# Optimization experiments

Hardware: AMD Instinct MI355X
Metric: run time of the kernel (lower is better)

Reference implementation:

```python
import jax, jax.numpy as jnp
import numpy as np

DIM = 1280
N_HEADS = 10
HEAD_DIM = 128
BASE = 10000.0
BATCH = 2
SEQ = 2048


def _rope(x):
    # x: [b, h, s, d]; matches source: split even/odd channels, rotate, concat halves
    b, h, s, d = x.shape
    theta = 1.0 / (BASE ** (jnp.arange(0, d, 2, dtype=jnp.float32) / d))  # [d/2]
    ang = jnp.arange(s, dtype=jnp.float32)[:, None] * theta               # [s, d/2]
    cos = jnp.cos(ang)
    sin = jnp.sin(ang)
    x1 = x[..., 0::2]
    x2 = x[..., 1::2]
    return jnp.concatenate([x1 * cos - x2 * sin, x1 * sin + x2 * cos], axis=-1)


def setup_inputs() -> dict:
    key = jax.random.key(0)
    ks = jax.random.split(key, 6)
    w_std = 0.02
    x = jax.random.normal(ks[0], (BATCH, SEQ, DIM), dtype=jnp.float32)
    positions = jnp.arange(SEQ, dtype=jnp.int64 if jax.config.jax_enable_x64 else jnp.int32)
    Wq = jax.random.normal(ks[1], (DIM, DIM), dtype=jnp.float32) * w_std
    Wk = jax.random.normal(ks[2], (DIM, DIM), dtype=jnp.float32) * w_std
    Wv = jax.random.normal(ks[3], (DIM, DIM), dtype=jnp.float32) * w_std
    Wo = jax.random.normal(ks[4], (DIM, DIM), dtype=jnp.float32) * w_std
    bq = jnp.zeros((DIM,), jnp.float32)
    bk = jnp.zeros((DIM,), jnp.float32)
    bv = jnp.zeros((DIM,), jnp.float32)
    bo = jnp.zeros((DIM,), jnp.float32)
    return {"x": x, "positions": positions, "Wq": Wq, "bq": bq, "Wk": Wk,
            "bk": bk, "Wv": Wv, "bv": bv, "Wo": Wo, "bo": bo}


def reference(x, positions, Wq, bq, Wk, bk, Wv, bv, Wo, bo):
    b, s, _ = x.shape
    scale = 1.0 / np.sqrt(HEAD_DIM)

    def proj(W, bias):
        y = jnp.einsum('bsd,ed->bse', x, W) + bias  # Linear: x @ W^T + b
        return y.reshape(b, s, N_HEADS, HEAD_DIM).transpose(0, 2, 1, 3)

    q = _rope(proj(Wq, bq))  # [b, h, s, hd]
    k = _rope(proj(Wk, bk))
    v = proj(Wv, bv)

    scores = jnp.einsum('bhqd,bhkd->bhqk', q, k) * scale
    causal = jnp.tril(jnp.ones((s, s), dtype=bool))
    scores = jnp.where(causal, scores, jnp.float32(-jnp.inf))
    attn = jax.nn.softmax(scores, axis=-1)
    out = jnp.einsum('bhqk,bhkd->bhqd', attn, v)
    out = out.transpose(0, 2, 1, 3).reshape(b, s, N_HEADS * HEAD_DIM)
    return jnp.einsum('bse,de->bsd', out, Wo) + bo
```

## Files before the change

kernel.cpp:

```cpp
#include <hip/hip_runtime.h>
#include <cmath>

typedef unsigned short u16;
typedef __attribute__((ext_vector_type(8))) short bf16x8;
typedef __attribute__((ext_vector_type(4))) float f32x4;

#define B_    2
#define SEQ_  2048
#define NH_   10
#define HD_   128
#define DIM_  1280

__device__ __forceinline__ u16 f2bf(float f) {
    union { float f; unsigned u; } v; v.f = f;
    unsigned r = (v.u + 0x7fffu + ((v.u >> 16) & 1u)) >> 16;
    return (u16)r;
}
__device__ __forceinline__ float bf2f(u16 h) {
    union { unsigned u; float f; } v; v.u = ((unsigned)h) << 16;
    return v.f;
}
__device__ __forceinline__ f32x4 mfma16(bf16x8 a, bf16x8 b, f32x4 c) {
    return __builtin_amdgcn_mfma_f32_16x16x32_bf16(a, b, c, 0, 0, 0);
}
__device__ __forceinline__ void g2l16(const void* g, void* l) {
    __builtin_amdgcn_global_load_lds(
        (const __attribute__((address_space(1))) unsigned*)g,
        (__attribute__((address_space(3))) unsigned*)l, 16, 0, 0);
}
__device__ __forceinline__ ushort4 pack4(float a, float b, float c, float d) {
    ushort4 w; w.x = f2bf(a); w.y = f2bf(b); w.z = f2bf(c); w.w = f2bf(d);
    return w;
}
__device__ __forceinline__ bf16x8 ldsr128(unsigned byte_off) {
    bf16x8 r;
    asm volatile("ds_read_b128 %0, %1" : "=v"(r) : "v"(byte_off));
    return r;
}
__device__ __forceinline__ unsigned lds_off(const void* p) {
    return (unsigned)(unsigned long long)
        (__attribute__((address_space(3))) const void*)p;
}

#define LGKM0() do { asm volatile("s_waitcnt lgkmcnt(0)" ::: "memory"); \
                     __builtin_amdgcn_sched_barrier(0); } while (0)
#define VMC(n)  asm volatile("s_waitcnt vmcnt(" #n ")" ::: "memory")

__global__ __launch_bounds__(256) void cvt_k(const float* __restrict__ x,
                                             const float* __restrict__ w0,
                                             const float* __restrict__ w1,
                                             const float* __restrict__ w2,
                                             const float* __restrict__ w3,
                                             u16* __restrict__ xb,
                                             u16* __restrict__ d0,
                                             u16* __restrict__ d1,
                                             u16* __restrict__ d2,
                                             u16* __restrict__ d3,
                                             float* __restrict__ ct,
                                             float* __restrict__ st) {
    const int NX = B_ * SEQ_ * DIM_;
    const int WN = DIM_ * DIM_;
    const int NCV = (NX + 4 * WN) / 8 / 256;
    int bid = blockIdx.x;
    if (bid >= NCV) {
        int idx = (bid - NCV) * 256 + threadIdx.x;
        int s = idx >> 6, j = idx & 63;
        float e = (float)j * (1.0f / 64.0f);
        float theta = 1.0f / powf(10000.0f, e);
        float ang = (float)s * theta;
        ct[idx] = cosf(ang);
        st[idx] = sinf(ang);
        return;
    }
    int i = (bid * 256 + threadIdx.x) * 8;
    const float* src; u16* dst; int off;
    if (i < NX) { src = x; dst = xb; off = i; }
    else {
        int j = i - NX; int w = j / WN; off = j - w * WN;
        src = (w == 0) ? w0 : (w == 1) ? w1 : (w == 2) ? w2 : w3;
        dst = (w == 0) ? d0 : (w == 1) ? d1 : (w == 2) ? d2 : d3;
    }
    float4 a0 = *(const float4*)(src + off);
    float4 a1 = *(const float4*)(src + off + 4);
    union { uint4 q; u16 u[8]; } t;
    t.u[0] = f2bf(a0.x); t.u[1] = f2bf(a0.y);
    t.u[2] = f2bf(a0.z); t.u[3] = f2bf(a0.w);
    t.u[4] = f2bf(a1.x); t.u[5] = f2bf(a1.y);
    t.u[6] = f2bf(a1.z); t.u[7] = f2bf(a1.w);
    *(uint4*)(dst + off) = t.q;
}

template <typename OT>
__device__ __forceinline__ void gemm_core(const u16* __restrict__ A,
                                          const u16* __restrict__ W,
                                          const float* __restrict__ bias,
                                          OT* __restrict__ C,
                                          int m_blk, int n_blk,
                                          u16* As, u16* Bs) {
    const int tid = threadIdx.x;
    const int wave = tid >> 6, lane = tid & 63;
    const int quad = lane >> 4, l16 = lane & 15;
    const int w_m = (wave >> 1) * 64, w_n = (wave & 1) * 64;
    const int srow = wave * 32;
    const int lrow = lane >> 3;
    const int csw = ((lane & 7) ^ lrow) * 8;
    const int rsw = l16 & 7;
    f32x4 acc[4][4] = {};

    const u16* pa = A + (size_t)(m_blk + srow + lrow) * DIM_ + csw;
    const u16* pb = W + (size_t)(n_blk + srow + lrow) * DIM_ + csw;

    for (int k0 = 0; k0 < DIM_; k0 += 64) {
        #pragma unroll
        for (int i = 0; i < 4; ++i) {
            g2l16(pa + k0 + i * 8 * DIM_, As + (srow + i * 8) * 64);
            g2l16(pb + k0 + i * 8 * DIM_, Bs + (srow + i * 8) * 64);
        }
        __syncthreads();
        #pragma unroll
        for (int kk = 0; kk < 2; ++kk) {
            bf16x8 af[4], bf[4];
            #pragma unroll
            for (int mt = 0; mt < 4; ++mt)
                af[mt] = *(const bf16x8*)&As[(w_m + mt * 16 + l16) * 64
                                             + ((kk * 4 + quad) ^ rsw) * 8];
            #pragma unroll
            for (int nt = 0; nt < 4; ++nt)
                bf[nt] = *(const bf16x8*)&Bs[(w_n + nt * 16 + l16) * 64
                                             + ((kk * 4 + quad) ^ rsw) * 8];
            #pragma unroll
            for (int mt = 0; mt < 4; ++mt)
                #pragma unroll
                for (int nt = 0; nt < 4; ++nt)
                    acc[mt][nt] = mfma16(af[mt], bf[nt], acc[mt][nt]);
        }
        __syncthreads();
    }
    #pragma unroll
    for (int nt = 0; nt < 4; ++nt) {
        int col = n_blk + w_n + nt * 16 + l16;
        float bv = bias[col];
        #pragma unroll
        for (int mt = 0; mt < 4; ++mt) {
            #pragma unroll
            for (int r = 0; r < 4; ++r) {
                int row = m_blk + w_m + mt * 16 + quad * 4 + r;
                float v = acc[mt][nt][r] + bv;
                if constexpr (sizeof(OT) == 4) C[(size_t)row * DIM_ + col] = v;
                else C[(size_t)row * DIM_ + col] = (OT)f2bf(v);
            }
        }
    }
}

__device__ __forceinline__ void gemm256_core(const u16* __restrict__ A,
                                             const u16* __restrict__ W,
                                             const float* __restrict__ bias,
                                             u16* __restrict__ C,
                                             int m_blk, int n_blk,
                                             u16* sm) {
    const int tid = threadIdx.x;
    const int wave = tid >> 6, lane = tid & 63;
    const int quad = lane >> 4, l16 = lane & 15;
    const int wr = wave >> 2, wc = wave & 3;
    const int rsw = (l16 >> 1) & 3;
    const unsigned smb = lds_off(sm);
    const unsigned aB = smb + ((wr * 128 + l16) * 32 + (quad ^ rsw) * 8) * 2;
    const unsigned bB = smb + (16384 + (wc * 64 + l16) * 32 + (quad ^ rsw) * 8) * 2;
    const int csw = ((lane & 3) ^ ((lane >> 3) & 3)) * 8;
    const int jA = wave * 2, jB = wave * 2 + 1;
    const int kkA = jA >> 3, gA0 = jA & 7;
    const int kkB = jB >> 3, gB0 = jB & 7;
    const u16* pa = A + (size_t)(m_blk + (lane >> 2)) * DIM_ + csw;
    const u16* pb = W + (size_t)(n_blk + (lane >> 2)) * DIM_ + csw;

    #define STG(p, mat, d, h, tk) do {                                        \
        int g0_ = gA0 + (h) * 8, g1_ = gB0 + (h) * 8;                         \
        g2l16((p) + (size_t)(g0_ * 16) * DIM_ + (tk) * 64 + kkA * 32,         \
              sm + (d) * 32768 + (mat) * 16384 + kkA * 8192 + g0_ * 512);     \
        g2l16((p) + (size_t)(g1_ * 16) * DIM_ + (tk) * 64 + kkB * 32,         \
              sm + (d) * 32768 + (mat) * 16384 + kkB * 8192 + g1_ * 512);     \
    } while (0)

    f32x4 acc[8][4] = {};
    bf16x8 b[2][4];

    STG(pa, 0, 0, 0, 0); STG(pa, 0, 0, 1, 0);
    STG(pb, 1, 0, 0, 0); STG(pb, 1, 0, 1, 0);
    STG(pb, 1, 1, 0, 1); STG(pb, 1, 1, 1, 1);
    VMC(4);
    asm volatile("s_waitcnt lgkmcnt(0)" ::: "memory");
    __builtin_amdgcn_s_barrier();

    const int NT = DIM_ / 64;
    for (int t = 0; t < NT; ++t) {
        const unsigned cu2 = (unsigned)(t & 1) * 65536u;
        const int d = t & 1;
        const bool sa = (t + 1 < NT), sb = (t + 2 < NT);
        const unsigned aT = aB + cu2, bT = bB + cu2;
        #pragma unroll
        for (int q = 0; q < 4; ++q) {
            if (q == 0) {
                #pragma unroll
                for (int kk = 0; kk < 2; ++kk)
                    #pragma unroll
                    for (int nt = 0; nt < 4; ++nt)
                        b[kk][nt] = ldsr128(bT + (kk * 8192 + nt * 512) * 2);
            }
            bf16x8 af[2][2];
            #pragma unroll
            for (int j = 0; j < 2; ++j)
                #pragma unroll
                for (int kk = 0; kk < 2; ++kk)
                    af[j][kk] = ldsr128(aT + ((2 * q + j) * 512 + kk * 8192) * 2);
            if (q == 0 && sa) STG(pa, 0, d ^ 1, 0, t + 1);
            if (q == 1 && sa) STG(pa, 0, d ^ 1, 1, t + 1);
            if (q == 2 && sb) STG(pb, 1, d, 0, t + 2);
            if (q == 3 && sb) STG(pb, 1, d, 1, t + 2);
            if (q == 0)
                asm volatile("s_waitcnt lgkmcnt(8)" ::: "memory");
            __builtin_amdgcn_s_barrier();
            LGKM0();
            __builtin_amdgcn_s_setprio(1);
            #pragma unroll
            for (int j = 0; j < 2; ++j)
                #pragma unroll
                for (int nt = 0; nt < 4; ++nt) {
                    acc[2 * q + j][nt] = mfma16(af[j][0], b[0][nt], acc[2 * q + j][nt]);
                    acc[2 * q + j][nt] = mfma16(af[j][1], b[1][nt], acc[2 * q + j][nt]);
                }
            __builtin_amdgcn_s_setprio(0);
            if (q == 3) {
                if (sb) VMC(4);
                else if (sa) VMC(0);
            }
            __builtin_amdgcn_s_barrier();
        }
    }
    #undef STG
    #pragma unroll
    for (int nt = 0; nt < 4; ++nt) {
        int col = n_blk + wc * 64 + nt * 16 + l16;
        float bv = bias[col];
        #pragma unroll
        for (int mt = 0; mt < 8; ++mt) {
            int row = m_blk + wr * 128 + mt * 16 + quad * 4;
            #pragma unroll
            for (int r = 0; r < 4; ++r)
                C[(size_t)(row + r) * DIM_ + col] = f2bf(acc[mt][nt][r] + bv);
        }
    }
}

__global__ __launch_bounds__(512, 2) void qkv_gemm(const u16* __restrict__ xb,
                                                   const u16* __restrict__ Wqb,
                                                   const u16* __restrict__ Wkb,
                                                   const u16* __restrict__ Wvb,
                                                   const float* __restrict__ bq,
                                                   const float* __restrict__ bk,
                                                   const float* __restrict__ bv,
                                                   u16* __restrict__ Qb,
                                                   u16* __restrict__ Kb,
                                                   u16* __restrict__ Vb) {
    __shared__ alignas(16) u16 sm[65536];
    int id = blockIdx.x;
    int xcd = id & 7, pid = id >> 3;
    int m = xcd * 2 + pid / 15;
    int ns = pid % 15;
    int wsel = ns / 5, n_blk = (ns % 5) * 256;
    const u16* W = (wsel == 0) ? Wqb : (wsel == 1) ? Wkb : Wvb;
    const float* bias = (wsel == 0) ? bq : (wsel == 1) ? bk : bv;
    u16* C = (wsel == 0) ? Qb : (wsel == 1) ? Kb : Vb;
    gemm256_core(xb, W, bias, C, m * 256, n_blk, sm);
}

__global__ __launch_bounds__(256) void out_gemm(const u16* __restrict__ AO,
                                                const u16* __restrict__ Wob,
                                                const float* __restrict__ bo,
                                                float* __restrict__ C) {
    __shared__ alignas(16) u16 As[128 * 64];
    __shared__ alignas(16) u16 Bs[128 * 64];
    int id = blockIdx.x;
    int xcd = id & 7, pid = id >> 3;
    int n = pid % 10;
    int m = xcd * 4 + pid / 10;
    gemm_core<float>(AO, Wob, bo, C, m * 128, n * 128, As, Bs);
}

__global__ __launch_bounds__(256) void rope_k(const u16* __restrict__ Qs_,
                                              const u16* __restrict__ Ks_,
                                              u16* __restrict__ Qd,
                                              u16* __restrict__ Kp,
                                              const float* __restrict__ ct,
                                              const float* __restrict__ st,
                                              float qscale) {
    int t = blockIdx.x * 256 + threadIdx.x;
    const int NR = B_ * SEQ_ * NH_;
    int rid = t >> 3, j0 = (t & 7) * 8;
    const bool isQ = (rid < NR);
    const u16* src = isQ ? Qs_ : Ks_;
    float sc = isQ ? qscale : 1.0f;
    if (!isQ) rid -= NR;
    int h = rid % NH_;
    int s = (rid / NH_) % SEQ_;
    int b = rid / (NH_ * SEQ_);
    const u16* p = src + (size_t)rid * HD_ + 2 * j0;
    union { uint4 q; u16 u[8]; } a0, a1, o1, o2;
    a0.q = *(const uint4*)p;
    a1.q = *(const uint4*)(p + 8);
    const float* cc = ct + (size_t)s * 64 + j0;
    const float* ss = st + (size_t)s * 64 + j0;
    #pragma unroll
    for (int j = 0; j < 8; ++j) {
        float x1 = bf2f((j < 4) ? a0.u[2 * j] : a1.u[2 * j - 8]);
        float x2 = bf2f((j < 4) ? a0.u[2 * j + 1] : a1.u[2 * j - 7]);
        float c = cc[j], sn = ss[j];
        o1.u[j] = f2bf((x1 * c - x2 * sn) * sc);
        o2.u[j] = f2bf((x1 * sn + x2 * c) * sc);
    }
    if (isQ) {
        u16* q = Qd + (size_t)(((size_t)b * SEQ_ + s) * NH_ + h) * HD_;
        *(uint4*)(q + j0) = o1.q;
        *(uint4*)(q + 64 + j0) = o2.q;
    } else {
        int kt = s >> 6, key = s & 63, nt = key >> 4, l16k = key & 15;
        int qd = (j0 >> 3) & 3;
        int kk1 = j0 >> 5, kk2 = 2 + kk1;
        u16* tb = Kp + ((size_t)((b * NH_ + h) * 32 + kt)) * 8192;
        int lane = qd * 16 + l16k;
        *(uint4*)(tb + (kk1 * 4 + nt) * 512 + lane * 8) = o1.q;
        *(uint4*)(tb + (kk2 * 4 + nt) * 512 + lane * 8) = o2.q;
    }
}

__global__ __launch_bounds__(256) void transpose_v(const u16* __restrict__ V,
                                                   u16* __restrict__ Vp) {
    __shared__ u16 T[128][72];
    int stile = blockIdx.x, h = blockIdx.y, b = blockIdx.z;
    int tid = threadIdx.x;
    {
        int sl = tid >> 2, d0 = (tid & 3) * 32;
        const u16* vp = V + ((size_t)((b * SEQ_ + stile * 64 + sl) * NH_ + h)) * HD_ + d0;
        #pragma unroll
        for (int i = 0; i < 4; ++i) {
            union { uint4 q; u16 u[8]; } r;
            r.q = *(const uint4*)(vp + i * 8);
            #pragma unroll
            for (int j = 0; j < 8; ++j) T[d0 + i * 8 + j][sl] = r.u[j];
        }
    }
    __syncthreads();
    {
        int d = tid >> 1, kc = (tid & 1) * 32;
        int dt = d >> 4, l16v = d & 15, kk = kc >> 5;
        u16* tb = Vp + ((size_t)((b * NH_ + h) * 32 + stile)) * 8192 + (kk * 8 + dt) * 512;
        #pragma unroll
        for (int i = 0; i < 4; ++i)
            *(uint4*)(tb + (i * 16 + l16v) * 8) = *(const uint4*)&T[d][kc + i * 8];
    }
}

__device__ const unsigned char QT_TAB[40] =
    {0,1,2,3,4,4,5,5,6,6,7,7,8,8,8,9,9,9,10,10,10,11,11,11,
     12,12,12,12,13,13,13,13,14,14,14,14,15,15,15,15};
__device__ const unsigned char CH_TAB[40] =
    {0,0,0,0,0,1,0,1,0,1,0,1,0,1,2,0,1,2,0,1,2,0,1,2,
     0,1,2,3,0,1,2,3,0,1,2,3,0,1,2,3};

__global__ __launch_bounds__(256, 3) void attn_k(const u16* __restrict__ Q,
                                                 const u16* __restrict__ Kp,
                                                 const u16* __restrict__ Vp,
                                                 u16* __restrict__ AO,
                                                 u16* __restrict__ PO,
                                                 float* __restrict__ Pl) {
    const int cid = blockIdx.x, h = blockIdx.y, b = blockIdx.z;
    const int qt = QT_TAB[cid], c = CH_TAB[cid];
    const int ntiles = 2 * qt + 2;
    const int nch = (ntiles + 7) >> 3;
    const int kt0 = c * 8;
    const int kt1 = (kt0 + 8 < ntiles) ? kt0 + 8 : ntiles;
    const int bh = b * NH_ + h;

    const int tid = threadIdx.x, wave = tid >> 6, lane = tid & 63;
    const int quad = lane >> 4, l16 = lane & 15;

    __shared__ alignas(16) u16 Ks[16 * 512];
    __shared__ alignas(16) u16 Vs[16 * 512];
    __shared__ alignas(16) u16 Pt[4][4][512];

    bf16x8 qf[2][4];
    #pragma unroll
    for (int mt = 0; mt < 2; ++mt) {
        int sq = qt * 128 + wave * 32 + mt * 16 + l16;
        const u16* qp = Q + ((size_t)((b * SEQ_ + sq) * NH_ + h)) * HD_;
        #pragma unroll
        for (int kk = 0; kk < 4; ++kk)
            qf[mt][kk] = *(const bf16x8*)(qp + kk * 32 + quad * 8);
    }
    f32x4 oacc[2][8] = {};
    float l_run[2] = {0.f, 0.f};
    const int q0 = qt * 128 + wave * 32 + l16;

    const u16* kpb = Kp + ((size_t)bh * 32) * 8192;
    const u16* vpb = Vp + ((size_t)bh * 32) * 8192;

    for (int kt = kt0; kt < kt1; ++kt) {
        const u16* kp_t = kpb + (size_t)kt * 8192;
        const u16* vp_t = vpb + (size_t)kt * 8192;
        #pragma unroll
        for (int i = 0; i < 4; ++i) {
            int f = wave * 4 + i;
            g2l16(kp_t + f * 512 + lane * 8, &Ks[f * 512]);
            g2l16(vp_t + f * 512 + lane * 8, &Vs[f * 512]);
        }
        __syncthreads();
        f32x4 sacc[2][4] = {};
        #pragma unroll
        for (int kk = 0; kk < 4; ++kk) {
            #pragma unroll
            for (int nt = 0; nt < 4; ++nt) {
                bf16x8 kf = *(const bf16x8*)&Ks[(kk * 4 + nt) * 512 + lane * 8];
                sacc[0][nt] = mfma16(kf, qf[0][kk], sacc[0][nt]);
                sacc[1][nt] = mfma16(kf, qf[1][kk], sacc[1][nt]);
            }
        }
        const bool maskt = (kt >= 2 * qt);
        const int keyb = kt * 64 + quad * 4;
        #pragma unroll
        for (int mt = 0; mt < 2; ++mt) {
            const int qg = q0 + mt * 16;
            float ps = 0.f;
            #pragma unroll
            for (int nt = 0; nt < 4; ++nt) {
                float p[4];
                #pragma unroll
                for (int r = 0; r < 4; ++r) {
                    float x = sacc[mt][nt][r] - 32.0f;
                    if (maskt && (keyb + nt * 16 + r > qg)) x = -INFINITY;
                    p[r] = __builtin_amdgcn_exp2f(x);
                    ps += p[r];
                }
                ushort4 w4 = pack4(p[0], p[1], p[2], p[3]);
                int rowf = (((nt & 1) << 1) | (quad >> 1)) * 16 + l16;
                *(ushort4*)&Pt[wave][mt * 2 + (nt >> 1)][rowf * 8 + (quad & 1) * 4] = w4;
            }
            l_run[mt] += ps;
        }
        #pragma unroll
        for (int kk = 0; kk < 2; ++kk) {
            bf16x8 pf0 = *(const bf16x8*)&Pt[wave][kk][(quad * 16 + l16) * 8];
            bf16x8 pf1 = *(const bf16x8*)&Pt[wave][2 + kk][(quad * 16 + l16) * 8];
            #pragma unroll
            for (int dt = 0; dt < 8; ++dt) {
                bf16x8 vf = *(const bf16x8*)&Vs[(kk * 8 + dt) * 512 + lane * 8];
                oacc[0][dt] = mfma16(vf, pf0, oacc[0][dt]);
                oacc[1][dt] = mfma16(vf, pf1, oacc[1][dt]);
            }
        }
        __syncthreads();
    }
    #pragma unroll
    for (int mt = 0; mt < 2; ++mt) {
        l_run[mt] += __shfl_xor(l_run[mt], 16, 64);
        l_run[mt] += __shfl_xor(l_run[mt], 32, 64);
    }
    if (nch == 1) {
        #pragma unroll
        for (int mt = 0; mt < 2; ++mt) {
            float invl = 1.0f / l_run[mt];
            int sq = q0 + mt * 16;
            u16* op = AO + ((size_t)((b * SEQ_ + sq) * NH_ + h)) * HD_ + quad * 4;
            #pragma unroll
            for (int dt = 0; dt < 8; ++dt) {
                ushort4 w4 = pack4(oacc[mt][dt][0] * invl, oacc[mt][dt][1] * invl,
                                   oacc[mt][dt][2] * invl, oacc[mt][dt][3] * invl);
                *(ushort4*)(op + dt * 16) = w4;
            }
        }
    } else {
        size_t pidx = ((size_t)bh * 16 + qt) * 4 + c;
        u16* po = PO + pidx * 16384;
        #pragma unroll
        for (int mt = 0; mt < 2; ++mt) {
            #pragma unroll
            for (int dt = 0; dt < 8; ++dt) {
                ushort4 w4 = pack4(oacc[mt][dt][0], oacc[mt][dt][1],
                                   oacc[mt][dt][2], oacc[mt][dt][3]);
                *(ushort4*)(po + ((wave * 16 + mt * 8 + dt) * 64 + lane) * 4) = w4;
            }
            if (quad == 0)
                Pl[pidx * 128 + wave * 32 + mt * 16 + l16] = l_run[mt];
        }
    }
}

__global__ __launch_bounds__(256) void combine_k(const u16* __restrict__ PO,
                                                 const float* __restrict__ Pl,
                                                 u16* __restrict__ AO) {
    const int qt = 4 + blockIdx.x, h = blockIdx.y, b = blockIdx.z;
    const int nch = (2 * qt + 2 + 7) >> 3;
    const int bh = b * NH_ + h;
    const int tid = threadIdx.x;
    const int q = tid >> 1, dh = tid & 1;
    const int wave = q >> 5, mt = (q >> 4) & 1, l16 = q & 15;
    size_t base = ((size_t)bh * 16 + qt) * 4;

    float L = 0.f;
    for (int c = 0; c < nch; ++c) L += Pl[(base + c) * 128 + q];
    float o[64];
    #pragma unroll
    for (int j = 0; j < 64; ++j) o[j] = 0.f;
    for (int c = 0; c < nch; ++c) {
        const u16* p = PO + (base + c) * 16384;
        #pragma unroll
        for (int dtl = 0; dtl < 4; ++dtl) {
            int dt = dh * 4 + dtl;
            #pragma unroll
            for (int quad = 0; quad < 4; ++quad) {
                union { ushort4 v; u16 u[4]; } t;
                t.v = *(const ushort4*)(p + ((wave * 16 + mt * 8 + dt) * 64
                                             + quad * 16 + l16) * 4);
                #pragma unroll
                for (int r = 0; r < 4; ++r)
                    o[dtl * 16 + quad * 4 + r] += bf2f(t.u[r]);
            }
        }
    }
    float invL = 1.0f / L;
    int sq = qt * 128 + q;
    u16* op = AO + ((size_t)((b * SEQ_ + sq) * NH_ + h)) * HD_ + dh * 64;
    union { uint4 v[8]; u16 u[64]; } t;
    #pragma unroll
    for (int j = 0; j < 64; ++j) t.u[j] = f2bf(o[j] * invL);
    #pragma unroll
    for (int i = 0; i < 8; ++i) *(uint4*)(op + i * 8) = t.v[i];
}

extern "C" void kernel_launch(void* const* d_in, const int* in_sizes, int n_in,
                              void* d_out, int out_size, void* d_ws, size_t ws_size,
                              hipStream_t stream) {
    const float* x  = (const float*)d_in[0];
    const float* Wq = (const float*)d_in[2];
    const float* bq = (const float*)d_in[3];
    const float* Wk = (const float*)d_in[4];
    const float* bk = (const float*)d_in[5];
    const float* Wv = (const float*)d_in[6];
    const float* bv = (const float*)d_in[7];
    const float* Wo = (const float*)d_in[8];
    const float* bo = (const float*)d_in[9];
    float* out = (float*)d_out;

    const size_t NE = (size_t)B_ * SEQ_ * NH_ * HD_;
    const size_t WN = (size_t)DIM_ * DIM_;
    u16* Qb  = (u16*)d_ws;
    u16* Kb  = Qb + NE;
    u16* Vb  = Kb + NE;
    u16* Vp  = Vb + NE;
    u16* xb  = Vp + NE;
    u16* Wqb = xb + NE;
    u16* Wkb = Wqb + WN;
    u16* Wvb = Wkb + WN;
    u16* Wob = Wvb + WN;
    float* ct = (float*)(Wob + WN);
    float* st = ct + (size_t)SEQ_ * 64;
    u16* PO  = (u16*)(st + (size_t)SEQ_ * 64);
    float* Pl = (float*)(PO + (size_t)B_ * NH_ * 16 * 4 * 16384);
    u16* Qr = Vb;
    u16* Kp = xb;
    u16* AO = Qb;

    const int NCVT = (B_ * SEQ_ * DIM_ + 4 * (int)WN) / 8 / 256;
    cvt_k<<<NCVT + 512, 256, 0, stream>>>(x, Wq, Wk, Wv, Wo,
                                          xb, Wqb, Wkb, Wvb, Wob, ct, st);

    qkv_gemm<<<dim3(240), 512, 0, stream>>>(xb, Wqb, Wkb, Wvb, bq, bk, bv,
                                            Qb, Kb, Vb);

    transpose_v<<<dim3(SEQ_ / 64, NH_, B_), 256, 0, stream>>>(Vb, Vp);

    const float qsc = 0.08838834764831845f * 1.4426950408889634f;
    rope_k<<<(2 * B_ * SEQ_ * NH_ * 8) / 256, 256, 0, stream>>>(Qb, Kb, Qr, Kp,
                                                                ct, st, qsc);

    attn_k<<<dim3(40, NH_, B_), 256, 0, stream>>>(Qr, Kp, Vp, AO, PO, Pl);
    combine_k<<<dim3(12, NH_, B_), 256, 0, stream>>>(PO, Pl, AO);

    out_gemm<<<dim3(320), 256, 0, stream>>>(AO, Wob, bo, out);
}
```

Measured before the change: 248.7 us.

## Double-buffer LDS tiles in output GEMM and attention kernel

Adds ping-pong shared-memory buffers to the output-projection GEMM and the attention kernel, so the next K/V (or A/W) tile is prefetched while the current one is used by MFMA. This removes one barrier per iteration and is meant to hide global-to-LDS load latency behind compute. In exchange LDS use doubles and the occupancy hints drop from 3 to 2 blocks for attention and are set to 2 for the GEMM, which could lose latency hiding through fewer resident waves.

```diff
diff --git a/kernel.cpp b/kernel.cpp
--- a/kernel.cpp
+++ b/kernel.cpp
@@ -91,12 +91,12 @@
 }
 
 template <typename OT>
-__device__ __forceinline__ void gemm_core(const u16* __restrict__ A,
-                                          const u16* __restrict__ W,
-                                          const float* __restrict__ bias,
-                                          OT* __restrict__ C,
-                                          int m_blk, int n_blk,
-                                          u16* As, u16* Bs) {
+__device__ __forceinline__ void gemm_core_db(const u16* __restrict__ A,
+                                             const u16* __restrict__ W,
+                                             const float* __restrict__ bias,
+                                             OT* __restrict__ C,
+                                             int m_blk, int n_blk,
+                                             u16* As, u16* Bs) {
     const int tid = threadIdx.x;
     const int wave = tid >> 6, lane = tid & 63;
     const int quad = lane >> 4, l16 = lane & 15;
@@ -110,24 +110,37 @@
     const u16* pa = A + (size_t)(m_blk + srow + lrow) * DIM_ + csw;
     const u16* pb = W + (size_t)(n_blk + srow + lrow) * DIM_ + csw;
 
+    #pragma unroll
+    for (int i = 0; i < 4; ++i) {
+        g2l16(pa + i * 8 * DIM_, As + (srow + i * 8) * 64);
+        g2l16(pb + i * 8 * DIM_, Bs + (srow + i * 8) * 64);
+    }
+    __syncthreads();
+    int cur = 0;
     for (int k0 = 0; k0 < DIM_; k0 += 64) {
-        #pragma unroll
-        for (int i = 0; i < 4; ++i) {
-            g2l16(pa + k0 + i * 8 * DIM_, As + (srow + i * 8) * 64);
-            g2l16(pb + k0 + i * 8 * DIM_, Bs + (srow + i * 8) * 64);
-        }
-        __syncthreads();
+        const int nxt = cur ^ 1;
+        if (k0 + 64 < DIM_) {
+            #pragma unroll
+            for (int i = 0; i < 4; ++i) {
+                g2l16(pa + k0 + 64 + i * 8 * DIM_,
+                      As + nxt * 8192 + (srow + i * 8) * 64);
+                g2l16(pb + k0 + 64 + i * 8 * DIM_,
+                      Bs + nxt * 8192 + (srow + i * 8) * 64);
+            }
+        }
+        const u16* Asc = As + cur * 8192;
+        const u16* Bsc = Bs + cur * 8192;
         #pragma unroll
         for (int kk = 0; kk < 2; ++kk) {
             bf16x8 af[4], bf[4];
             #pragma unroll
             for (int mt = 0; mt < 4; ++mt)
-                af[mt] = *(const bf16x8*)&As[(w_m + mt * 16 + l16) * 64
-                                             + ((kk * 4 + quad) ^ rsw) * 8];
+                af[mt] = *(const bf16x8*)&Asc[(w_m + mt * 16 + l16) * 64
+                                              + ((kk * 4 + quad) ^ rsw) * 8];
             #pragma unroll
             for (int nt = 0; nt < 4; ++nt)
-                bf[nt] = *(const bf16x8*)&Bs[(w_n + nt * 16 + l16) * 64
-                                             + ((kk * 4 + quad) ^ rsw) * 8];
+                bf[nt] = *(const bf16x8*)&Bsc[(w_n + nt * 16 + l16) * 64
+                                              + ((kk * 4 + quad) ^ rsw) * 8];
             #pragma unroll
             for (int mt = 0; mt < 4; ++mt)
                 #pragma unroll
@@ -135,6 +148,7 @@
                     acc[mt][nt] = mfma16(af[mt], bf[nt], acc[mt][nt]);
         }
         __syncthreads();
+        cur = nxt;
     }
     #pragma unroll
     for (int nt = 0; nt < 4; ++nt) {
@@ -274,17 +288,17 @@
     gemm256_core(xb, W, bias, C, m * 256, n_blk, sm);
 }
 
-__global__ __launch_bounds__(256) void out_gemm(const u16* __restrict__ AO,
-                                                const u16* __restrict__ Wob,
-                                                const float* __restrict__ bo,
-                                                float* __restrict__ C) {
-    __shared__ alignas(16) u16 As[128 * 64];
-    __shared__ alignas(16) u16 Bs[128 * 64];
+__global__ __launch_bounds__(256, 2) void out_gemm(const u16* __restrict__ AO,
+                                                   const u16* __restrict__ Wob,
+                                                   const float* __restrict__ bo,
+                                                   float* __restrict__ C) {
+    __shared__ alignas(16) u16 As[2 * 128 * 64];
+    __shared__ alignas(16) u16 Bs[2 * 128 * 64];
     int id = blockIdx.x;
     int xcd = id & 7, pid = id >> 3;
     int n = pid % 10;
     int m = xcd * 4 + pid / 10;
-    gemm_core<float>(AO, Wob, bo, C, m * 128, n * 128, As, Bs);
+    gemm_core_db<float>(AO, Wob, bo, C, m * 128, n * 128, As, Bs);
 }
 
 __global__ __launch_bounds__(256) void rope_k(const u16* __restrict__ Qs_,
@@ -367,7 +381,7 @@
     {0,0,0,0,0,1,0,1,0,1,0,1,0,1,2,0,1,2,0,1,2,0,1,2,
      0,1,2,3,0,1,2,3,0,1,2,3,0,1,2,3};
 
-__global__ __launch_bounds__(256, 3) void attn_k(const u16* __restrict__ Q,
+__global__ __launch_bounds__(256, 2) void attn_k(const u16* __restrict__ Q,
                                                  const u16* __restrict__ Kp,
                                                  const u16* __restrict__ Vp,
                                                  u16* __restrict__ AO,
@@ -384,8 +398,8 @@
     const int tid = threadIdx.x, wave = tid >> 6, lane = tid & 63;
     const int quad = lane >> 4, l16 = lane & 15;
 
-    __shared__ alignas(16) u16 Ks[16 * 512];
-    __shared__ alignas(16) u16 Vs[16 * 512];
+    __shared__ alignas(16) u16 Ks[2][16 * 512];
+    __shared__ alignas(16) u16 Vs[2][16 * 512];
     __shared__ alignas(16) u16 Pt[4][4][512];
 
     bf16x8 qf[2][4];
@@ -404,22 +418,35 @@
     const u16* kpb = Kp + ((size_t)bh * 32) * 8192;
     const u16* vpb = Vp + ((size_t)bh * 32) * 8192;
 
-    for (int kt = kt0; kt < kt1; ++kt) {
-        const u16* kp_t = kpb + (size_t)kt * 8192;
-        const u16* vp_t = vpb + (size_t)kt * 8192;
+    {
+        const u16* kp_t = kpb + (size_t)kt0 * 8192;
+        const u16* vp_t = vpb + (size_t)kt0 * 8192;
         #pragma unroll
         for (int i = 0; i < 4; ++i) {
             int f = wave * 4 + i;
-            g2l16(kp_t + f * 512 + lane * 8, &Ks[f * 512]);
-            g2l16(vp_t + f * 512 + lane * 8, &Vs[f * 512]);
-        }
-        __syncthreads();
+            g2l16(kp_t + f * 512 + lane * 8, &Ks[0][f * 512]);
+            g2l16(vp_t + f * 512 + lane * 8, &Vs[0][f * 512]);
+        }
+    }
+    __syncthreads();
+    int cur = 0;
+    for (int kt = kt0; kt < kt1; ++kt) {
+        if (kt + 1 < kt1) {
+            const u16* kp_n = kpb + (size_t)(kt + 1) * 8192;
+            const u16* vp_n = vpb + (size_t)(kt + 1) * 8192;
+            #pragma unroll
+            for (int i = 0; i < 4; ++i) {
+                int f = wave * 4 + i;
+                g2l16(kp_n + f * 512 + lane * 8, &Ks[cur ^ 1][f * 512]);
+                g2l16(vp_n + f * 512 + lane * 8, &Vs[cur ^ 1][f * 512]);
+            }
+        }
         f32x4 sacc[2][4] = {};
         #pragma unroll
         for (int kk = 0; kk < 4; ++kk) {
             #pragma unroll
             for (int nt = 0; nt < 4; ++nt) {
-                bf16x8 kf = *(const bf16x8*)&Ks[(kk * 4 + nt) * 512 + lane * 8];
+                bf16x8 kf = *(const bf16x8*)&Ks[cur][(kk * 4 + nt) * 512 + lane * 8];
                 sacc[0][nt] = mfma16(kf, qf[0][kk], sacc[0][nt]);
                 sacc[1][nt] = mfma16(kf, qf[1][kk], sacc[1][nt]);
             }
@@ -452,12 +479,13 @@
             bf16x8 pf1 = *(const bf16x8*)&Pt[wave][2 + kk][(quad * 16 + l16) * 8];
             #pragma unroll
             for (int dt = 0; dt < 8; ++dt) {
-                bf16x8 vf = *(const bf16x8*)&Vs[(kk * 8 + dt) * 512 + lane * 8];
+                bf16x8 vf = *(const bf16x8*)&Vs[cur][(kk * 8 + dt) * 512 + lane * 8];
                 oacc[0][dt] = mfma16(vf, pf0, oacc[0][dt]);
                 oacc[1][dt] = mfma16(vf, pf1, oacc[1][dt]);
             }
         }
         __syncthreads();
+        cur ^= 1;
     }
     #pragma unroll
     for (int mt = 0; mt < 2; ++mt) {
```

Result: no change. 249.8 us (+0.5%).

## Fuse Q RoPE into attention and use hardware packed bf16 conversion

Applied to the files above, without the earlier changes.

Applies the query rotary embedding and softmax scale inside the attention kernel while loading Q fragments, so the standalone RoPE kernel only handles K. This removes one read and write pass over Q and one scratch buffer. Software bf16 rounding is replaced with the v_cvt_pk_bf16_f32 instruction in several kernels to cut ALU work. The fixed -32 offset before exp2 is dropped. The attention output now aliases the raw Q buffer that blocks are still reading, which risks a read/write race between blocks that share a query tile.

```diff
diff --git a/kernel.cpp b/kernel.cpp
--- a/kernel.cpp
+++ b/kernel.cpp
@@ -20,6 +20,11 @@
     union { unsigned u; float f; } v; v.u = ((unsigned)h) << 16;
     return v.f;
 }
+__device__ __forceinline__ unsigned cvt2(float lo, float hi) {
+    unsigned r;
+    asm("v_cvt_pk_bf16_f32 %0, %1, %2" : "=v"(r) : "v"(lo), "v"(hi));
+    return r;
+}
 __device__ __forceinline__ f32x4 mfma16(bf16x8 a, bf16x8 b, f32x4 c) {
     return __builtin_amdgcn_mfma_f32_16x16x32_bf16(a, b, c, 0, 0, 0);
 }
@@ -29,8 +34,10 @@
         (__attribute__((address_space(3))) unsigned*)l, 16, 0, 0);
 }
 __device__ __forceinline__ ushort4 pack4(float a, float b, float c, float d) {
-    ushort4 w; w.x = f2bf(a); w.y = f2bf(b); w.z = f2bf(c); w.w = f2bf(d);
-    return w;
+    union { ushort4 w; unsigned u[2]; } r;
+    r.u[0] = cvt2(a, b);
+    r.u[1] = cvt2(c, d);
+    return r.w;
 }
 __device__ __forceinline__ bf16x8 ldsr128(unsigned byte_off) {
     bf16x8 r;
@@ -82,11 +89,11 @@
     }
     float4 a0 = *(const float4*)(src + off);
     float4 a1 = *(const float4*)(src + off + 4);
-    union { uint4 q; u16 u[8]; } t;
-    t.u[0] = f2bf(a0.x); t.u[1] = f2bf(a0.y);
-    t.u[2] = f2bf(a0.z); t.u[3] = f2bf(a0.w);
-    t.u[4] = f2bf(a1.x); t.u[5] = f2bf(a1.y);
-    t.u[6] = f2bf(a1.z); t.u[7] = f2bf(a1.w);
+    union { uint4 q; unsigned w[4]; } t;
+    t.w[0] = cvt2(a0.x, a0.y);
+    t.w[1] = cvt2(a0.z, a0.w);
+    t.w[2] = cvt2(a1.x, a1.y);
+    t.w[3] = cvt2(a1.z, a1.w);
     *(uint4*)(dst + off) = t.q;
 }
 
@@ -287,50 +294,43 @@
     gemm_core<float>(AO, Wob, bo, C, m * 128, n * 128, As, Bs);
 }
 
-__global__ __launch_bounds__(256) void rope_k(const u16* __restrict__ Qs_,
-                                              const u16* __restrict__ Ks_,
-                                              u16* __restrict__ Qd,
+__global__ __launch_bounds__(256) void rope_k(const u16* __restrict__ Ks_,
                                               u16* __restrict__ Kp,
                                               const float* __restrict__ ct,
-                                              const float* __restrict__ st,
-                                              float qscale) {
+                                              const float* __restrict__ st) {
     int t = blockIdx.x * 256 + threadIdx.x;
-    const int NR = B_ * SEQ_ * NH_;
     int rid = t >> 3, j0 = (t & 7) * 8;
-    const bool isQ = (rid < NR);
-    const u16* src = isQ ? Qs_ : Ks_;
-    float sc = isQ ? qscale : 1.0f;
-    if (!isQ) rid -= NR;
     int h = rid % NH_;
     int s = (rid / NH_) % SEQ_;
     int b = rid / (NH_ * SEQ_);
-    const u16* p = src + (size_t)rid * HD_ + 2 * j0;
-    union { uint4 q; u16 u[8]; } a0, a1, o1, o2;
+    const u16* p = Ks_ + (size_t)rid * HD_ + 2 * j0;
+    union { uint4 q; u16 u[8]; } a0, a1;
     a0.q = *(const uint4*)p;
     a1.q = *(const uint4*)(p + 8);
     const float* cc = ct + (size_t)s * 64 + j0;
     const float* ss = st + (size_t)s * 64 + j0;
+    float y1[8], y2[8];
     #pragma unroll
     for (int j = 0; j < 8; ++j) {
         float x1 = bf2f((j < 4) ? a0.u[2 * j] : a1.u[2 * j - 8]);
         float x2 = bf2f((j < 4) ? a0.u[2 * j + 1] : a1.u[2 * j - 7]);
         float c = cc[j], sn = ss[j];
-        o1.u[j] = f2bf((x1 * c - x2 * sn) * sc);
-        o2.u[j] = f2bf((x1 * sn + x2 * c) * sc);
-    }
-    if (isQ) {
-        u16* q = Qd + (size_t)(((size_t)b * SEQ_ + s) * NH_ + h) * HD_;
-        *(uint4*)(q + j0) = o1.q;
-        *(uint4*)(q + 64 + j0) = o2.q;
-    } else {
-        int kt = s >> 6, key = s & 63, nt = key >> 4, l16k = key & 15;
-        int qd = (j0 >> 3) & 3;
-        int kk1 = j0 >> 5, kk2 = 2 + kk1;
-        u16* tb = Kp + ((size_t)((b * NH_ + h) * 32 + kt)) * 8192;
-        int lane = qd * 16 + l16k;
-        *(uint4*)(tb + (kk1 * 4 + nt) * 512 + lane * 8) = o1.q;
-        *(uint4*)(tb + (kk2 * 4 + nt) * 512 + lane * 8) = o2.q;
-    }
+        y1[j] = x1 * c - x2 * sn;
+        y2[j] = x1 * sn + x2 * c;
+    }
+    union { uint4 q; unsigned w[4]; } o1, o2;
+    #pragma unroll
+    for (int p2 = 0; p2 < 4; ++p2) {
+        o1.w[p2] = cvt2(y1[2 * p2], y1[2 * p2 + 1]);
+        o2.w[p2] = cvt2(y2[2 * p2], y2[2 * p2 + 1]);
+    }
+    int kt = s >> 6, key = s & 63, nt = key >> 4, l16k = key & 15;
+    int qd = (j0 >> 3) & 3;
+    int kk1 = j0 >> 5, kk2 = 2 + kk1;
+    u16* tb = Kp + ((size_t)((b * NH_ + h) * 32 + kt)) * 8192;
+    int lane = qd * 16 + l16k;
+    *(uint4*)(tb + (kk1 * 4 + nt) * 512 + lane * 8) = o1.q;
+    *(uint4*)(tb + (kk2 * 4 + nt) * 512 + lane * 8) = o2.q;
 }
 
 __global__ __launch_bounds__(256) void transpose_v(const u16* __restrict__ V,
@@ -367,12 +367,15 @@
     {0,0,0,0,0,1,0,1,0,1,0,1,0,1,2,0,1,2,0,1,2,0,1,2,
      0,1,2,3,0,1,2,3,0,1,2,3,0,1,2,3};
 
-__global__ __launch_bounds__(256, 3) void attn_k(const u16* __restrict__ Q,
+__global__ __launch_bounds__(256, 3) void attn_k(const u16* Q,
                                                  const u16* __restrict__ Kp,
                                                  const u16* __restrict__ Vp,
-                                                 u16* __restrict__ AO,
+                                                 u16* AO,
                                                  u16* __restrict__ PO,
-                                                 float* __restrict__ Pl) {
+                                                 float* __restrict__ Pl,
+                                                 const float* __restrict__ ct,
+                                                 const float* __restrict__ st,
+                                                 float qsc) {
     const int cid = blockIdx.x, h = blockIdx.y, b = blockIdx.z;
     const int qt = QT_TAB[cid], c = CH_TAB[cid];
     const int ntiles = 2 * qt + 2;
@@ -393,10 +396,34 @@
     for (int mt = 0; mt < 2; ++mt) {
         int sq = qt * 128 + wave * 32 + mt * 16 + l16;
         const u16* qp = Q + ((size_t)((b * SEQ_ + sq) * NH_ + h)) * HD_;
-        #pragma unroll
-        for (int kk = 0; kk < 4; ++kk)
-            qf[mt][kk] = *(const bf16x8*)(qp + kk * 32 + quad * 8);
-    }
+        const float* cc = ct + (size_t)sq * 64;
+        const float* ss = st + (size_t)sq * 64;
+        #pragma unroll
+        for (int kk = 0; kk < 2; ++kk) {
+            const int j0 = kk * 32 + quad * 8;
+            union { uint4 q4; u16 u[8]; } r0, r1;
+            r0.q4 = *(const uint4*)(qp + 2 * j0);
+            r1.q4 = *(const uint4*)(qp + 2 * j0 + 8);
+            float y1[8], y2[8];
+            #pragma unroll
+            for (int j = 0; j < 8; ++j) {
+                float x1 = bf2f((j < 4) ? r0.u[2 * j] : r1.u[2 * j - 8]);
+                float x2 = bf2f((j < 4) ? r0.u[2 * j + 1] : r1.u[2 * j - 7]);
+                float cv = cc[j0 + j], sv = ss[j0 + j];
+                y1[j] = (x1 * cv - x2 * sv) * qsc;
+                y2[j] = (x1 * sv + x2 * cv) * qsc;
+            }
+            union { bf16x8 v; unsigned w[4]; } o1, o2;
+            #pragma unroll
+            for (int p2 = 0; p2 < 4; ++p2) {
+                o1.w[p2] = cvt2(y1[2 * p2], y1[2 * p2 + 1]);
+                o2.w[p2] = cvt2(y2[2 * p2], y2[2 * p2 + 1]);
+            }
+            qf[mt][kk] = o1.v;
+            qf[mt][kk + 2] = o2.v;
+        }
+    }
+
     f32x4 oacc[2][8] = {};
     float l_run[2] = {0.f, 0.f};
     const int q0 = qt * 128 + wave * 32 + l16;
@@ -435,7 +462,7 @@
                 float p[4];
                 #pragma unroll
                 for (int r = 0; r < 4; ++r) {
-                    float x = sacc[mt][nt][r] - 32.0f;
+                    float x = sacc[mt][nt][r];
                     if (maskt && (keyb + nt * 16 + r > qg)) x = -INFINITY;
                     p[r] = __builtin_amdgcn_exp2f(x);
                     ps += p[r];
@@ -529,9 +556,10 @@
     float invL = 1.0f / L;
     int sq = qt * 128 + q;
     u16* op = AO + ((size_t)((b * SEQ_ + sq) * NH_ + h)) * HD_ + dh * 64;
-    union { uint4 v[8]; u16 u[64]; } t;
-    #pragma unroll
-    for (int j = 0; j < 64; ++j) t.u[j] = f2bf(o[j] * invL);
+    union { uint4 v[8]; unsigned w[32]; } t;
+    #pragma unroll
+    for (int j = 0; j < 32; ++j)
+        t.w[j] = cvt2(o[2 * j] * invL, o[2 * j + 1] * invL);
     #pragma unroll
     for (int i = 0; i < 8; ++i) *(uint4*)(op + i * 8) = t.v[i];
 }
@@ -565,7 +593,6 @@
     float* st = ct + (size_t)SEQ_ * 64;
     u16* PO  = (u16*)(st + (size_t)SEQ_ * 64);
     float* Pl = (float*)(PO + (size_t)B_ * NH_ * 16 * 4 * 16384);
-    u16* Qr = Vb;
     u16* Kp = xb;
     u16* AO = Qb;
 
@@ -578,11 +605,11 @@
 
     transpose_v<<<dim3(SEQ_ / 64, NH_, B_), 256, 0, stream>>>(Vb, Vp);
 
+    rope_k<<<(B_ * SEQ_ * NH_ * 8) / 256, 256, 0, stream>>>(Kb, Kp, ct, st);
+
     const float qsc = 0.08838834764831845f * 1.4426950408889634f;
-    rope_k<<<(2 * B_ * SEQ_ * NH_ * 8) / 256, 256, 0, stream>>>(Qb, Kb, Qr, Kp,
-                                                                ct, st, qsc);
-
-    attn_k<<<dim3(40, NH_, B_), 256, 0, stream>>>(Qr, Kp, Vp, AO, PO, Pl);
+    attn_k<<<dim3(40, NH_, B_), 256, 0, stream>>>(Qb, Kp, Vp, AO, PO, Pl,
+                                                  ct, st, qsc);
     combine_k<<<dim3(12, NH_, B_), 256, 0, stream>>>(PO, Pl, AO);
 
     out_gemm<<<dim3(320), 256, 0, stream>>>(AO, Wob, bo, out);
```

New measurement: 258.1 us. +3.8%, slower.
